# Kernel tuning notes

Measured on AMD Instinct MI355X. Metric: run time of the kernel, lower is better.

## Reference

```python
import jax, jax.numpy as jnp
import numpy as np

N_ATOMS = 131072
N_TYPES = 256
D_IN = 64
D_OUT = 64


def setup_inputs() -> dict:
    key = jax.random.key(0)
    k_x, k_t, k_w, k_b = jax.random.split(key, 4)
    x = jax.random.normal(k_x, (N_ATOMS, D_IN), dtype=jnp.float32)
    atom_types = jax.random.randint(k_t, (N_ATOMS,), 0, N_TYPES, dtype=jnp.int64)
    # Per-atom-type linear weights/biases (the 'unique' table gathered per atom).
    W = jax.random.normal(k_w, (N_TYPES, D_OUT, D_IN), dtype=jnp.float32) * (1.0 / np.sqrt(D_IN))
    b = jax.random.normal(k_b, (N_TYPES, D_OUT), dtype=jnp.float32) * 0.01
    return {"x": x, "atom_types": atom_types, "W": W, "b": b}


def reference(x, atom_types, W, b):
    # Gather type-specific linear params per atom (gather_unique_first semantics),
    # apply the per-atom linear, then tanh.
    Wg = W[atom_types]          # [N, d_out, d_in]
    bg = b[atom_types]          # [N, d_out]
    y = jnp.einsum('noi,ni->no', Wg, x) + bg  # [N, d_out]
    return jnp.tanh(y)
```

## Files before the change

### kernel.cpp

```cpp
#include <hip/hip_runtime.h>

#define N_ATOMS 131072
#define N_TYPES 256
#define D 64
#define CAP 1024
#define BPT 4
#define G_BLK (N_ATOMS / 1024)
#define IDX_MASK (N_ATOMS - 1)

using sfrag = __attribute__((ext_vector_type(8))) short;
using ffrag = __attribute__((ext_vector_type(4))) float;

__device__ __forceinline__ short f2bf(float f)
{
    union { float f; unsigned u; } v; v.f = f;
    unsigned r = v.u + 0x7FFFu + ((v.u >> 16) & 1u);
    return (short)(r >> 16);
}

__device__ __forceinline__ float fast_tanh(float v)
{
    float e = __expf(2.0f * v);
    return 1.0f - __fdividef(2.0f, e + 1.0f);
}

__global__ __launch_bounds__(256) void hist_kernel(
    const int* __restrict__ types, int* __restrict__ bhist)
{
    __shared__ int lhist[N_TYPES];
    const int tid  = threadIdx.x;
    const int base = blockIdx.x * 1024;
    lhist[tid] = 0;
    __syncthreads();

    int ty[4];
#pragma unroll
    for (int k = 0; k < 4; ++k) ty[k] = types[base + k * 256 + tid];
#pragma unroll
    for (int k = 0; k < 4; ++k) atomicAdd(&lhist[ty[k]], 1);
    __syncthreads();

    bhist[blockIdx.x * N_TYPES + tid] = lhist[tid];
}

__global__ __launch_bounds__(256) void scatter_kernel(
    const int* __restrict__ types, const int* __restrict__ bhist,
    int* __restrict__ cursor, int* __restrict__ bucket)
{
    __shared__ int lbase[N_TYPES];
    __shared__ int lcur[N_TYPES];
    const int tid  = threadIdx.x;
    const int blk  = blockIdx.x;
    const int base = blk * 1024;

    int s = 0;
#pragma unroll 8
    for (int b = 0; b < blk; ++b) s += bhist[b * N_TYPES + tid];
    lbase[tid] = s;
    lcur[tid]  = 0;
    if (blk == G_BLK - 1) cursor[tid] = s + bhist[(G_BLK - 1) * N_TYPES + tid];
    __syncthreads();

    int ty[4];
#pragma unroll
    for (int k = 0; k < 4; ++k) ty[k] = types[base + k * 256 + tid];
#pragma unroll
    for (int k = 0; k < 4; ++k) {
        const int t = ty[k];
        const int p = atomicAdd(&lcur[t], 1);
        const int q = lbase[t] + p;
        if (q < CAP) bucket[t * CAP + q] = base + k * 256 + tid;
    }
}

__global__ __launch_bounds__(256, 4) void apply_kernel(
    const float* __restrict__ x, const float* __restrict__ W,
    const float* __restrict__ b, const int* __restrict__ bucket,
    const int* __restrict__ cursor, float* __restrict__ out)
{
    const int t = blockIdx.x & 255;
    const int j = blockIdx.x >> 8;
    const int wave = threadIdx.x >> 6;
    const int lane = threadIdx.x & 63;
    const int c = lane & 15;
    const int q = lane >> 4;

    const int*   bk = bucket + (size_t)t * CAP;
    const float* Wt = W + (size_t)t * (D * D);

    const int g0 = j * 4 + wave;
    const int g1 = g0 + 16;

    int i0 = bk[g0 * 16 + c] & IDX_MASK;
    int i1 = bk[g1 * 16 + c] & IDX_MASK;

    const float4* xr0 = (const float4*)x + (size_t)i0 * 16 + q * 2;
    float4 a00 = xr0[0], a01 = xr0[1], a02 = xr0[8], a03 = xr0[9];
    const float4* xr1 = (const float4*)x + (size_t)i1 * 16 + q * 2;
    float4 a10 = xr1[0], a11 = xr1[1], a12 = xr1[8], a13 = xr1[9];

    sfrag Bf[4][2];
#pragma unroll
    for (int nt = 0; nt < 4; ++nt) {
#pragma unroll
        for (int ks = 0; ks < 2; ++ks) {
            const float4* wr = (const float4*)(Wt + (size_t)(nt * 16 + c) * D + ks * 32 + q * 8);
            float4 w0 = wr[0], w1 = wr[1];
            sfrag f;
            f[0] = f2bf(w0.x); f[1] = f2bf(w0.y); f[2] = f2bf(w0.z); f[3] = f2bf(w0.w);
            f[4] = f2bf(w1.x); f[5] = f2bf(w1.y); f[6] = f2bf(w1.z); f[7] = f2bf(w1.w);
            Bf[nt][ks] = f;
        }
    }
    float bias[4];
#pragma unroll
    for (int nt = 0; nt < 4; ++nt) bias[nt] = b[(size_t)t * D + nt * 16 + c];

    int n = cursor[t];
    if (n > CAP) n = CAP;

    auto compute = [&](int g, int aidx, float4 x0, float4 x1, float4 x2, float4 x3) {
        sfrag A0, A1;
        A0[0] = f2bf(x0.x); A0[1] = f2bf(x0.y); A0[2] = f2bf(x0.z); A0[3] = f2bf(x0.w);
        A0[4] = f2bf(x1.x); A0[5] = f2bf(x1.y); A0[6] = f2bf(x1.z); A0[7] = f2bf(x1.w);
        A1[0] = f2bf(x2.x); A1[1] = f2bf(x2.y); A1[2] = f2bf(x2.z); A1[3] = f2bf(x2.w);
        A1[4] = f2bf(x3.x); A1[5] = f2bf(x3.y); A1[6] = f2bf(x3.z); A1[7] = f2bf(x3.w);

        const int gb = g * 16;
        int  oat[4]; bool ov[4];
#pragma unroll
        for (int r = 0; r < 4; ++r) {
            ov[r]  = (gb + q * 4 + r) < n;
            oat[r] = __shfl(aidx, q * 4 + r, 64);
        }
#pragma unroll
        for (int nt = 0; nt < 4; ++nt) {
            ffrag acc = {0.f, 0.f, 0.f, 0.f};
            acc = __builtin_amdgcn_mfma_f32_16x16x32_bf16(A0, Bf[nt][0], acc, 0, 0, 0);
            acc = __builtin_amdgcn_mfma_f32_16x16x32_bf16(A1, Bf[nt][1], acc, 0, 0, 0);
#pragma unroll
            for (int r = 0; r < 4; ++r) {
                if (ov[r])
                    out[(size_t)oat[r] * D + nt * 16 + c] = fast_tanh(acc[r] + bias[nt]);
            }
        }
    };

    if (g0 * 16 < n) compute(g0, i0, a00, a01, a02, a03);
    if (g1 * 16 < n) compute(g1, i1, a10, a11, a12, a13);

    for (int g = g0 + 32; g * 16 < n; g += 16) {
        int ii = bk[g * 16 + c] & IDX_MASK;
        const float4* xr = (const float4*)x + (size_t)ii * 16 + q * 2;
        float4 b0 = xr[0], b1 = xr[1], b2 = xr[8], b3 = xr[9];
        compute(g, ii, b0, b1, b2, b3);
    }
}

extern "C" void kernel_launch(void* const* d_in, const int* in_sizes, int n_in,
                              void* d_out, int out_size, void* d_ws, size_t ws_size,
                              hipStream_t stream)
{
    const float* x     = (const float*)d_in[0];
    const int*   types = (const int*)  d_in[1];
    const float* W     = (const float*)d_in[2];
    const float* b     = (const float*)d_in[3];
    float*       out   = (float*)d_out;

    int* cursor = (int*)d_ws;
    int* bucket = (int*)((char*)d_ws + 1024);
    int* bhist  = (int*)((char*)d_ws + 1024 + (size_t)N_TYPES * CAP * sizeof(int));

    hist_kernel   <<<dim3(G_BLK), dim3(256), 0, stream>>>(types, bhist);
    scatter_kernel<<<dim3(G_BLK), dim3(256), 0, stream>>>(types, bhist, cursor, bucket);
    apply_kernel  <<<dim3(BPT * N_TYPES), dim3(256), 0, stream>>>(x, W, b, bucket, cursor, out);
}
```

Before: 108.3 us.

## Fuse histogram and scatter into one kernel with inter-block flag synchronization

Merges the histogram and scatter kernels into a single launch. Each block publishes its per-type counts and then spin-waits on release/acquire flags from all earlier blocks before computing its prefix offsets, which removes one kernel launch and the reload of types. Output stores in the apply kernel become nontemporal. The spin-wait relies on all 128 blocks being co-resident. Flags use a magic value and are never cleared, so a stale flag left in the workspace from a previous call could let a block read old counts.

```diff
diff --git a/kernel.cpp b/kernel.cpp
--- a/kernel.cpp
+++ b/kernel.cpp
@@ -7,6 +7,7 @@
 #define BPT 4
 #define G_BLK (N_ATOMS / 1024)
 #define IDX_MASK (N_ATOMS - 1)
+#define FLAG_MAGIC 0x13570000
 
 using sfrag = __attribute__((ext_vector_type(8))) short;
 using ffrag = __attribute__((ext_vector_type(4))) float;
@@ -24,12 +25,18 @@
     return 1.0f - __fdividef(2.0f, e + 1.0f);
 }
 
-__global__ __launch_bounds__(256) void hist_kernel(
-    const int* __restrict__ types, int* __restrict__ bhist)
+__global__ __launch_bounds__(256) void sort_kernel(
+    const int* __restrict__ types, int* __restrict__ bhist, int* __restrict__ flags,
+    int* __restrict__ cursor, int* __restrict__ bucket)
 {
+    __shared__ int lbase[N_TYPES];
+    __shared__ int lcur[N_TYPES];
     __shared__ int lhist[N_TYPES];
+
     const int tid  = threadIdx.x;
-    const int base = blockIdx.x * 1024;
+    const int blk  = blockIdx.x;
+    const int base = blk * 1024;
+
     lhist[tid] = 0;
     __syncthreads();
 
@@ -40,30 +47,30 @@
     for (int k = 0; k < 4; ++k) atomicAdd(&lhist[ty[k]], 1);
     __syncthreads();
 
-    bhist[blockIdx.x * N_TYPES + tid] = lhist[tid];
-}
+    const int cnt = lhist[tid];
+    bhist[blk * N_TYPES + tid] = cnt;
+    __threadfence();
+    __syncthreads();
+    if (tid == 0)
+        __hip_atomic_store(&flags[blk], FLAG_MAGIC | blk,
+                           __ATOMIC_RELEASE, __HIP_MEMORY_SCOPE_AGENT);
 
-__global__ __launch_bounds__(256) void scatter_kernel(
-    const int* __restrict__ types, const int* __restrict__ bhist,
-    int* __restrict__ cursor, int* __restrict__ bucket)
-{
-    __shared__ int lbase[N_TYPES];
-    __shared__ int lcur[N_TYPES];
-    const int tid  = threadIdx.x;
-    const int blk  = blockIdx.x;
-    const int base = blk * 1024;
+    if (tid < blk) {
+        while (__hip_atomic_load(&flags[tid], __ATOMIC_ACQUIRE,
+                                 __HIP_MEMORY_SCOPE_AGENT) != (FLAG_MAGIC | tid))
+            __builtin_amdgcn_s_sleep(1);
+    }
+    __syncthreads();
+    __threadfence();
 
     int s = 0;
 #pragma unroll 8
     for (int b = 0; b < blk; ++b) s += bhist[b * N_TYPES + tid];
     lbase[tid] = s;
     lcur[tid]  = 0;
-    if (blk == G_BLK - 1) cursor[tid] = s + bhist[(G_BLK - 1) * N_TYPES + tid];
+    if (blk == G_BLK - 1) cursor[tid] = s + cnt;
     __syncthreads();
 
-    int ty[4];
-#pragma unroll
-    for (int k = 0; k < 4; ++k) ty[k] = types[base + k * 256 + tid];
 #pragma unroll
     for (int k = 0; k < 4; ++k) {
         const int t = ty[k];
@@ -141,7 +148,8 @@
 #pragma unroll
             for (int r = 0; r < 4; ++r) {
                 if (ov[r])
-                    out[(size_t)oat[r] * D + nt * 16 + c] = fast_tanh(acc[r] + bias[nt]);
+                    __builtin_nontemporal_store(fast_tanh(acc[r] + bias[nt]),
+                        &out[(size_t)oat[r] * D + nt * 16 + c]);
             }
         }
     };
@@ -169,9 +177,10 @@
 
     int* cursor = (int*)d_ws;
     int* bucket = (int*)((char*)d_ws + 1024);
-    int* bhist  = (int*)((char*)d_ws + 1024 + (size_t)N_TYPES * CAP * sizeof(int));
+    int* bhist  = (int*)((char*)d_ws + 1024 + (size_t)N_TYPES * CAP * 4);
+    int* flags  = (int*)((char*)d_ws + 1024 + (size_t)N_TYPES * CAP * 4
+                                    + (size_t)G_BLK * N_TYPES * 4);
 
-    hist_kernel   <<<dim3(G_BLK), dim3(256), 0, stream>>>(types, bhist);
-    scatter_kernel<<<dim3(G_BLK), dim3(256), 0, stream>>>(types, bhist, cursor, bucket);
-    apply_kernel  <<<dim3(BPT * N_TYPES), dim3(256), 0, stream>>>(x, W, b, bucket, cursor, out);
+    sort_kernel <<<dim3(G_BLK),       dim3(256), 0, stream>>>(types, bhist, flags, cursor, bucket);
+    apply_kernel<<<dim3(BPT * N_TYPES), dim3(256), 0, stream>>>(x, W, b, bucket, cursor, out);
 }
```

New measurement: 125.6 us. +16.0%, slower.
